# Kernel optimization log

Measured on AMD Instinct MI355X. Metric: run time of the kernel, lower is better.

The kernel has to match this reference:

```python
import jax, jax.numpy as jnp
import numpy as np

SAMPLE_RATE = 44100.0


def _peaking_coeffs(freq, gain_db, q, fs):
    """RBJ cookbook peaking-EQ biquad coefficients (as in dasp-pytorch).
    freq/gain_db/q: [B, K]. Returns normalized b0,b1,b2,a1,a2 each [B, K]."""
    A = jnp.power(10.0, gain_db / 40.0)
    w0 = 2.0 * jnp.pi * freq / fs
    cosw = jnp.cos(w0)
    alpha = jnp.sin(w0) / (2.0 * q)
    b0 = 1.0 + alpha * A
    b1 = -2.0 * cosw
    b2 = 1.0 - alpha * A
    a0 = 1.0 + alpha / A
    a1 = -2.0 * cosw
    a2 = 1.0 - alpha / A
    inv_a0 = 1.0 / a0
    return b0 * inv_a0, b1 * inv_a0, b2 * inv_a0, a1 * inv_a0, a2 * inv_a0


def setup_inputs() -> dict:
    key = jax.random.key(0)
    k1, k2, k3, k4 = jax.random.split(key, 4)
    B, C, T, K = 32, 2, 262144, 6
    audio = jax.random.normal(k1, (B, C, T), dtype=jnp.float32) * 0.1
    # realistic EQ parameter ranges
    frequencies = 100.0 + jax.random.uniform(k2, (B, K), dtype=jnp.float32) * 9900.0  # 100 Hz .. 10 kHz
    gains = jax.random.normal(k3, (B, K), dtype=jnp.float32) * 6.0                     # ~ +/- 6 dB
    q_factors = 0.5 + jax.random.uniform(k4, (B, K), dtype=jnp.float32) * 3.0          # 0.5 .. 3.5
    return {"audio": audio, "frequencies": frequencies, "gains": gains, "q_factors": q_factors}


def reference(audio, frequencies, gains, q_factors):
    # audio: [B, C, T]; per-batch cascade of K peaking biquads over time.
    B, C, T = audio.shape
    K = frequencies.shape[1]
    b0, b1, b2, a1, a2 = _peaking_coeffs(frequencies, gains, q_factors, SAMPLE_RATE)
    # [K, B, 1] for broadcasting over channels
    b0, b1, b2, a1, a2 = (jnp.transpose(c)[:, :, None] for c in (b0, b1, b2, a1, a2))

    def step(carry, x):  # x: [B, C], one time sample through the whole cascade
        s1, s2 = carry  # each [K, B, C], direct-form II transposed states
        y = x
        ns1, ns2 = [], []
        for k in range(K):  # small fixed band loop (structurally sequential cascade)
            yk = b0[k] * y + s1[k]
            ns1.append(b1[k] * y - a1[k] * yk + s2[k])
            ns2.append(b2[k] * y - a2[k] * yk)
            y = yk
        return (jnp.stack(ns1), jnp.stack(ns2)), y

    init = (jnp.zeros((K, B, C), audio.dtype), jnp.zeros((K, B, C), audio.dtype))
    xs = jnp.moveaxis(audio, 2, 0)  # [T, B, C]
    _, ys = jax.lax.scan(step, init, xs)
    return jnp.moveaxis(ys, 0, 2)  # [B, C, T]
```

## Files before the change

kernel.cpp:

```cpp
#include <hip/hip_runtime.h>
#include <math.h>

namespace {
constexpr int B = 32, C = 2, T = 262144, K = 6;
constexpr int SEG = 2048;
constexpr int L = T / SEG;
constexpr int NBC = B * C;
constexpr int NST = 2 * K;
constexpr int LOG2L = 7;
constexpr int TS = 16;
constexpr int NT = L / TS;
constexpr int WPB = SEG / 64;
constexpr int GP = 8;
constexpr int NW = 4;
constexpr float FS = 44100.0f;
}

__device__ __forceinline__ float rl(float v, int lane) {
  return __int_as_float(__builtin_amdgcn_readlane(__float_as_int(v), lane));
}

__device__ __forceinline__ void ld12(const float* p, float (&v)[NST]) {
  const float4* q = reinterpret_cast<const float4*>(p);
  float4 a = q[0], b4 = q[1], c4 = q[2];
  v[0] = a.x; v[1] = a.y; v[2] = a.z; v[3] = a.w;
  v[4] = b4.x; v[5] = b4.y; v[6] = b4.z; v[7] = b4.w;
  v[8] = c4.x; v[9] = c4.y; v[10] = c4.z; v[11] = c4.w;
}

__device__ __forceinline__ void st12(float* p, const float (&v)[NST]) {
  float4* q = reinterpret_cast<float4*>(p);
  q[0] = make_float4(v[0], v[1], v[2], v[3]);
  q[1] = make_float4(v[4], v[5], v[6], v[7]);
  q[2] = make_float4(v[8], v[9], v[10], v[11]);
}

__device__ __forceinline__ void affine(const float (&M)[NST][NST], float (&s)[NST],
                                       const float (&z)[NST]) {
  float ns[NST];
#pragma unroll
  for (int r = 0; r < NST; ++r) {
    float a = z[r];
#pragma unroll
    for (int m = 0; m < NST; ++m) a = fmaf(M[r][m], s[m], a);
    ns[r] = a;
  }
#pragma unroll
  for (int r = 0; r < NST; ++r) s[r] = ns[r];
}

__device__ __forceinline__ void coeffs_for_b(const float* __restrict__ fr,
                                             const float* __restrict__ gn,
                                             const float* __restrict__ qf, int b,
                                             float (&cb0)[K], float (&cb1)[K],
                                             float (&cb2)[K], float (&ca1)[K],
                                             float (&ca2)[K]) {
#pragma unroll
  for (int k = 0; k < K; ++k) {
    float f = fr[b * K + k], g = gn[b * K + k], Q = qf[b * K + k];
    float A  = powf(10.0f, g * (1.0f / 40.0f));
    float w0 = 6.283185307179586f * f / FS;
    float cw = cosf(w0);
    float al = sinf(w0) / (2.0f * Q);
    float ia = 1.0f / (1.0f + al / A);
    cb0[k] = (1.0f + al * A) * ia;
    cb1[k] = (-2.0f * cw) * ia;
    cb2[k] = (1.0f - al * A) * ia;
    ca1[k] = (-2.0f * cw) * ia;
    ca2[k] = (1.0f - al / A) * ia;
  }
}

template <bool WRITE_OUT>
__global__ __launch_bounds__(64, 2) void eq_pass(const float* __restrict__ x,
                                                 const float* __restrict__ fr,
                                                 const float* __restrict__ gn,
                                                 const float* __restrict__ qf,
                                                 float* __restrict__ cf,
                                                 const float* __restrict__ st_in,
                                                 float* __restrict__ st_out,
                                                 float* __restrict__ y) {
  __shared__ float sIn[2][64][17];
  __shared__ float sOut[2][64][17];

  int l = threadIdx.x;
  int wid = blockIdx.x;
  int bc = wid / WPB;
  int segbase = (wid % WPB) * 64;
  int b = bc / C;
  int tid = bc * SEG + segbase + l;

  const float4* xp4 = reinterpret_cast<const float4*>(x + (size_t)bc * T + (size_t)segbase * L);
  float4* yp4 = reinterpret_cast<float4*>(y + (size_t)bc * T + (size_t)segbase * L);
  constexpr int Q4 = L / 4;

  int sj = l >> 2;
  int qj = l & 3;

  float4 ra[4], rb[4];
#pragma unroll
  for (int j = 0; j < 4; ++j) ra[j] = xp4[(size_t)(j * 16 + sj) * Q4 + qj];
#pragma unroll
  for (int j = 0; j < 4; ++j) rb[j] = xp4[(size_t)(j * 16 + sj) * Q4 + 4 + qj];

  float b0[K], b1c[K], b2c[K], a1c[K], a2c[K];
  if (!WRITE_OUT) {
    coeffs_for_b(fr, gn, qf, b, b0, b1c, b2c, a1c, a2c);
    if ((wid % (WPB * C)) == 0) {
#pragma unroll
      for (int k = 0; k < K; ++k) {
        if (l == k) {
          float* p = cf + (b * K + k) * 5;
          p[0] = b0[k]; p[1] = b1c[k]; p[2] = b2c[k]; p[3] = a1c[k]; p[4] = a2c[k];
        }
      }
    }
  } else {
#pragma unroll
    for (int k = 0; k < K; ++k) {
      const float* p = cf + (b * K + k) * 5;
      b0[k] = p[0]; b1c[k] = p[1]; b2c[k] = p[2]; a1c[k] = p[3]; a2c[k] = p[4];
    }
  }

  float s1[K], s2[K];
  if (WRITE_OUT) {
    float st[NST];
    ld12(st_in + (size_t)tid * NST, st);
#pragma unroll
    for (int k = 0; k < K; ++k) { s1[k] = st[2 * k]; s2[k] = st[2 * k + 1]; }
  } else {
#pragma unroll
    for (int k = 0; k < K; ++k) { s1[k] = 0.0f; s2[k] = 0.0f; }
  }

  auto tile = [&](float4 (&r)[4], int t, int pb) {
#pragma unroll
    for (int j = 0; j < 4; ++j) {
      int seg = j * 16 + sj;
      sIn[pb][seg][qj * 4 + 0] = r[j].x;
      sIn[pb][seg][qj * 4 + 1] = r[j].y;
      sIn[pb][seg][qj * 4 + 2] = r[j].z;
      sIn[pb][seg][qj * 4 + 3] = r[j].w;
    }
    if (t + 2 < NT) {
#pragma unroll
      for (int j = 0; j < 4; ++j)
        r[j] = xp4[(size_t)(j * 16 + sj) * Q4 + (size_t)(t + 2) * 4 + qj];
    }
    float out16[TS];
#pragma unroll
    for (int i = 0; i < TS; ++i) {
      float yv = sIn[pb][l][i];
#pragma unroll
      for (int k = 0; k < K; ++k) {
        float yk = fmaf(b0[k], yv, s1[k]);
        float t1 = fmaf(b1c[k], yv, s2[k]);
        s1[k] = fmaf(-a1c[k], yk, t1);
        float t2 = b2c[k] * yv;
        s2[k] = fmaf(-a2c[k], yk, t2);
        yv = yk;
      }
      out16[i] = yv;
    }
    if (WRITE_OUT) {
#pragma unroll
      for (int i = 0; i < TS; ++i) sOut[pb][l][i] = out16[i];
#pragma unroll
      for (int j = 0; j < 4; ++j) {
        int seg = j * 16 + sj;
        float4 o;
        o.x = sOut[pb][seg][qj * 4 + 0];
        o.y = sOut[pb][seg][qj * 4 + 1];
        o.z = sOut[pb][seg][qj * 4 + 2];
        o.w = sOut[pb][seg][qj * 4 + 3];
        yp4[(size_t)seg * Q4 + (size_t)t * 4 + qj] = o;
      }
    }
  };

  for (int tt = 0; tt < NT; tt += 2) {
    tile(ra, tt, 0);
    tile(rb, tt + 1, 1);
  }

  if (!WRITE_OUT) {
    float st[NST];
#pragma unroll
    for (int k = 0; k < K; ++k) { st[2 * k] = s1[k]; st[2 * k + 1] = s2[k]; }
    st12(st_out + (size_t)tid * NST, st);
  }
}

__global__ __launch_bounds__(256, 1) void eq_scan(const float* __restrict__ cf,
                                                  const float* __restrict__ zsf,
                                                  float* __restrict__ sif) {
  __shared__ float PhiL[NST][NST];
  __shared__ float Rg[NST][NST + 1];
  __shared__ float Rw[NST][NST + 1];
  __shared__ float FB[NW][64][NST + 1];
  __shared__ float SL[NW][64][NST + 1];
  __shared__ float WF[NW][NST + 1];

  int bc = blockIdx.x;
  int b = bc / C;
  int t = threadIdx.x;
  int w = t >> 6;
  int l = t & 63;
  bool act = (l < NST);

  float b0[K], b1c[K], b2c[K], a1c[K], a2c[K];
#pragma unroll
  for (int k = 0; k < K; ++k) {
    const float* p = cf + (b * K + k) * 5;
    b0[k] = p[0]; b1c[k] = p[1]; b2c[k] = p[2]; a1c[k] = p[3]; a2c[k] = p[4];
  }

  float col[NST];
  {
    float s1[K], s2[K];
#pragma unroll
    for (int k = 0; k < K; ++k) {
      s1[k] = (l == 2 * k) ? 1.0f : 0.0f;
      s2[k] = (l == 2 * k + 1) ? 1.0f : 0.0f;
    }
    float yv = 0.0f;
#pragma unroll
    for (int k = 0; k < K; ++k) {
      float yk = fmaf(b0[k], yv, s1[k]);
      float t1 = fmaf(b1c[k], yv, s2[k]);
      float ns1 = fmaf(-a1c[k], yk, t1);
      float ns2 = fmaf(-a2c[k], yk, b2c[k] * yv);
      s1[k] = ns1; s2[k] = ns2; yv = yk;
    }
#pragma unroll
    for (int k = 0; k < K; ++k) { col[2 * k] = s1[k]; col[2 * k + 1] = s2[k]; }
  }

  auto square = [&]() {
    float nc[NST];
#pragma unroll
    for (int r = 0; r < NST; ++r) nc[r] = 0.0f;
#pragma unroll
    for (int m = 0; m < NST; ++m) {
      float wv = col[m];
#pragma unroll
      for (int r = 0; r < NST; ++r) nc[r] = fmaf(rl(col[r], m), wv, nc[r]);
    }
#pragma unroll
    for (int r = 0; r < NST; ++r) col[r] = nc[r];
  };

  for (int p = 0; p < LOG2L; ++p) square();
  if (w == 0 && act) {
#pragma unroll
    for (int r = 0; r < NST; ++r) PhiL[r][l] = col[r];
  }
  for (int p = 0; p < 3; ++p) square();
  if (w == 0 && act) {
#pragma unroll
    for (int r = 0; r < NST; ++r) Rg[r][l] = col[r];
  }
  for (int p = 0; p < 6; ++p) square();
  if (w == 0 && act) {
#pragma unroll
    for (int r = 0; r < NST; ++r) Rw[r][l] = col[r];
  }
  __syncthreads();

  float rowg[NST], roww[NST];
#pragma unroll
  for (int m = 0; m < NST; ++m) {
    rowg[m] = act ? Rg[l][m] : 0.0f;
    roww[m] = act ? Rw[l][m] : 0.0f;
  }
  float phi[NST][NST];
#pragma unroll
  for (int r = 0; r < NST; ++r)
#pragma unroll
    for (int m = 0; m < NST; ++m) phi[r][m] = PhiL[r][m];

  const float* zb = zsf + ((size_t)bc * SEG + (size_t)t * GP) * NST;
  float s[NST];
  ld12(zb, s);
#pragma unroll
  for (int j = 1; j < GP; ++j) {
    float zc[NST];
    ld12(zb + (size_t)j * NST, zc);
    affine(phi, s, zc);
  }
#pragma unroll
  for (int r = 0; r < NST; ++r) FB[w][l][r] = s[r];
  __syncthreads();

  {
    float sv = 0.0f;
    for (int i = 0; i < 64; ++i) {
      float wv = act ? FB[w][i][l] : 0.0f;
      float t0 = fmaf(rowg[0], rl(sv, 0), fmaf(rowg[1], rl(sv, 1), rowg[2] * rl(sv, 2)));
      float t1 = fmaf(rowg[3], rl(sv, 3), fmaf(rowg[4], rl(sv, 4), rowg[5] * rl(sv, 5)));
      float t2 = fmaf(rowg[6], rl(sv, 6), fmaf(rowg[7], rl(sv, 7), rowg[8] * rl(sv, 8)));
      float t3 = fmaf(rowg[9], rl(sv, 9), fmaf(rowg[10], rl(sv, 10), rowg[11] * rl(sv, 11)));
      sv = ((t0 + t1) + (t2 + t3)) + wv;
    }
    if (act) WF[w][l] = sv;
  }
  __syncthreads();

  float swv = 0.0f;
  for (int w2 = 0; w2 < w; ++w2) {
    float wfv = act ? WF[w2][l] : 0.0f;
    float t0 = fmaf(roww[0], rl(swv, 0), fmaf(roww[1], rl(swv, 1), roww[2] * rl(swv, 2)));
    float t1 = fmaf(roww[3], rl(swv, 3), fmaf(roww[4], rl(swv, 4), roww[5] * rl(swv, 5)));
    float t2 = fmaf(roww[6], rl(swv, 6), fmaf(roww[7], rl(swv, 7), roww[8] * rl(swv, 8)));
    float t3 = fmaf(roww[9], rl(swv, 9), fmaf(roww[10], rl(swv, 10), roww[11] * rl(swv, 11)));
    swv = ((t0 + t1) + (t2 + t3)) + wfv;
  }

  {
    float sv = swv;
    for (int i = 0; i < 64; ++i) {
      if (act) SL[w][i][l] = sv;
      float wv = act ? FB[w][i][l] : 0.0f;
      float t0 = fmaf(rowg[0], rl(sv, 0), fmaf(rowg[1], rl(sv, 1), rowg[2] * rl(sv, 2)));
      float t1 = fmaf(rowg[3], rl(sv, 3), fmaf(rowg[4], rl(sv, 4), rowg[5] * rl(sv, 5)));
      float t2 = fmaf(rowg[6], rl(sv, 6), fmaf(rowg[7], rl(sv, 7), rowg[8] * rl(sv, 8)));
      float t3 = fmaf(rowg[9], rl(sv, 9), fmaf(rowg[10], rl(sv, 10), rowg[11] * rl(sv, 11)));
      sv = ((t0 + t1) + (t2 + t3)) + wv;
    }
  }
  __syncthreads();

  float sg[NST];
#pragma unroll
  for (int r = 0; r < NST; ++r) sg[r] = SL[w][l][r];
  float* ob = sif + ((size_t)bc * SEG + (size_t)t * GP) * NST;
#pragma unroll
  for (int j = 0; j < GP; ++j) {
    st12(ob + (size_t)j * NST, sg);
    if (j + 1 < GP) {
      float zc[NST];
      ld12(zb + (size_t)j * NST, zc);
      affine(phi, sg, zc);
    }
  }
}

extern "C" void kernel_launch(void* const* d_in, const int* in_sizes, int n_in,
                              void* d_out, int out_size, void* d_ws, size_t ws_size,
                              hipStream_t stream) {
  const float* audio = (const float*)d_in[0];
  const float* fr    = (const float*)d_in[1];
  const float* gn    = (const float*)d_in[2];
  const float* qf    = (const float*)d_in[3];
  float* out = (float*)d_out;

  float* cf  = (float*)d_ws;
  float* zsf = cf + B * K * 5;
  float* sif = zsf + (size_t)NBC * SEG * NST;

  hipLaunchKernelGGL((eq_pass<false>), dim3(NBC * WPB), dim3(64), 0, stream,
                     audio, fr, gn, qf, cf, nullptr, zsf, out);
  hipLaunchKernelGGL(eq_scan, dim3(NBC), dim3(256), 0, stream, cf, zsf, sif);
  hipLaunchKernelGGL((eq_pass<true>), dim3(NBC * WPB), dim3(64), 0, stream,
                     audio, fr, gn, qf, cf, sif, nullptr, out);
}
```

Measured before the change: 84.44 us.

## Fuse two-pass scan into single kernel with decoupled lookback across blocks

Replaces the three-kernel scheme (local pass writing per-segment states, a separate scan kernel, and a second pass) with a small prep kernel computing coefficients and transition-matrix powers, plus one fused kernel. Each block handles one chunk of a row, does the local zero-state pass, an in-block scan of segment states, and then waits on a flag from the previous chunk's block to chain inter-block carries before rerunning the filter and writing output. This removes the global write and read of all per-segment states and two kernel boundaries, but serializes chunks through spin-waiting flags and relies on all blocks of a row being co-resident to avoid stalls.

```diff
diff --git a/kernel.cpp b/kernel.cpp
--- a/kernel.cpp
+++ b/kernel.cpp
@@ -3,58 +3,48 @@
 
 namespace {
 constexpr int B = 32, C = 2, T = 262144, K = 6;
-constexpr int SEG = 2048;
-constexpr int L = T / SEG;
 constexpr int NBC = B * C;
 constexpr int NST = 2 * K;
-constexpr int LOG2L = 7;
+constexpr int PB = 8;
+constexpr int CH = T / PB;
+constexpr int NW = 4;
+constexpr int SEGL = CH / (NW * 64);
 constexpr int TS = 16;
-constexpr int NT = L / TS;
-constexpr int WPB = SEG / 64;
-constexpr int GP = 8;
-constexpr int NW = 4;
+constexpr int NT = SEGL / TS;
+constexpr int Q4 = SEGL / 4;
+constexpr int SQ1 = 7;
+constexpr int SQ2 = 6;
+constexpr int SQ3 = 2;
 constexpr float FS = 44100.0f;
+constexpr size_t OFF_CF = 0;
+constexpr size_t OFF_RL = 960;
+constexpr size_t OFF_RW = OFF_RL + 4608;
+constexpr size_t OFF_RC = OFF_RW + 4608;
+constexpr size_t OFF_ST = OFF_RC + 4608;
+constexpr size_t OFF_FL = OFF_ST + 6144;
 }
 
 __device__ __forceinline__ float rl(float v, int lane) {
   return __int_as_float(__builtin_amdgcn_readlane(__float_as_int(v), lane));
 }
 
-__device__ __forceinline__ void ld12(const float* p, float (&v)[NST]) {
-  const float4* q = reinterpret_cast<const float4*>(p);
-  float4 a = q[0], b4 = q[1], c4 = q[2];
-  v[0] = a.x; v[1] = a.y; v[2] = a.z; v[3] = a.w;
-  v[4] = b4.x; v[5] = b4.y; v[6] = b4.z; v[7] = b4.w;
-  v[8] = c4.x; v[9] = c4.y; v[10] = c4.z; v[11] = c4.w;
-}
-
-__device__ __forceinline__ void st12(float* p, const float (&v)[NST]) {
-  float4* q = reinterpret_cast<float4*>(p);
-  q[0] = make_float4(v[0], v[1], v[2], v[3]);
-  q[1] = make_float4(v[4], v[5], v[6], v[7]);
-  q[2] = make_float4(v[8], v[9], v[10], v[11]);
-}
-
-__device__ __forceinline__ void affine(const float (&M)[NST][NST], float (&s)[NST],
-                                       const float (&z)[NST]) {
-  float ns[NST];
-#pragma unroll
-  for (int r = 0; r < NST; ++r) {
-    float a = z[r];
-#pragma unroll
-    for (int m = 0; m < NST; ++m) a = fmaf(M[r][m], s[m], a);
-    ns[r] = a;
-  }
-#pragma unroll
-  for (int r = 0; r < NST; ++r) s[r] = ns[r];
-}
-
-__device__ __forceinline__ void coeffs_for_b(const float* __restrict__ fr,
-                                             const float* __restrict__ gn,
-                                             const float* __restrict__ qf, int b,
-                                             float (&cb0)[K], float (&cb1)[K],
-                                             float (&cb2)[K], float (&ca1)[K],
-                                             float (&ca2)[K]) {
+__device__ __forceinline__ float mv_step(const float (&row)[NST], float sv) {
+  float t0 = fmaf(row[0], rl(sv, 0), fmaf(row[1], rl(sv, 1), row[2] * rl(sv, 2)));
+  float t1 = fmaf(row[3], rl(sv, 3), fmaf(row[4], rl(sv, 4), row[5] * rl(sv, 5)));
+  float t2 = fmaf(row[6], rl(sv, 6), fmaf(row[7], rl(sv, 7), row[8] * rl(sv, 8)));
+  float t3 = fmaf(row[9], rl(sv, 9), fmaf(row[10], rl(sv, 10), row[11] * rl(sv, 11)));
+  return (t0 + t1) + (t2 + t3);
+}
+
+__global__ __launch_bounds__(64) void eq_prep(const float* __restrict__ fr,
+                                              const float* __restrict__ gn,
+                                              const float* __restrict__ qf,
+                                              float* __restrict__ ws) {
+  int b = blockIdx.x;
+  int l = threadIdx.x;
+  float* cf = ws + OFF_CF;
+
+  float cb0[K], cb1[K], cb2[K], ca1[K], ca2[K];
 #pragma unroll
   for (int k = 0; k < K; ++k) {
     float f = fr[b * K + k], g = gn[b * K + k], Q = qf[b * K + k];
@@ -69,280 +59,272 @@
     ca1[k] = (-2.0f * cw) * ia;
     ca2[k] = (1.0f - al / A) * ia;
   }
-}
-
-template <bool WRITE_OUT>
-__global__ __launch_bounds__(64, 2) void eq_pass(const float* __restrict__ x,
-                                                 const float* __restrict__ fr,
-                                                 const float* __restrict__ gn,
-                                                 const float* __restrict__ qf,
-                                                 float* __restrict__ cf,
-                                                 const float* __restrict__ st_in,
-                                                 float* __restrict__ st_out,
-                                                 float* __restrict__ y) {
-  __shared__ float sIn[2][64][17];
-  __shared__ float sOut[2][64][17];
-
-  int l = threadIdx.x;
-  int wid = blockIdx.x;
-  int bc = wid / WPB;
-  int segbase = (wid % WPB) * 64;
-  int b = bc / C;
-  int tid = bc * SEG + segbase + l;
-
-  const float4* xp4 = reinterpret_cast<const float4*>(x + (size_t)bc * T + (size_t)segbase * L);
-  float4* yp4 = reinterpret_cast<float4*>(y + (size_t)bc * T + (size_t)segbase * L);
-  constexpr int Q4 = L / 4;
-
-  int sj = l >> 2;
-  int qj = l & 3;
+#pragma unroll
+  for (int k = 0; k < K; ++k) {
+    if (l == k) {
+      float* p = cf + (b * K + k) * 5;
+      p[0] = cb0[k]; p[1] = cb1[k]; p[2] = cb2[k]; p[3] = ca1[k]; p[4] = ca2[k];
+    }
+  }
+
+  float col[NST];
+  {
+    float s1[K], s2[K];
+#pragma unroll
+    for (int k = 0; k < K; ++k) {
+      s1[k] = (l == 2 * k) ? 1.0f : 0.0f;
+      s2[k] = (l == 2 * k + 1) ? 1.0f : 0.0f;
+    }
+    float yv = 0.0f;
+#pragma unroll
+    for (int k = 0; k < K; ++k) {
+      float yk = fmaf(cb0[k], yv, s1[k]);
+      float t1 = fmaf(cb1[k], yv, s2[k]);
+      float ns1 = fmaf(-ca1[k], yk, t1);
+      float ns2 = fmaf(-ca2[k], yk, cb2[k] * yv);
+      s1[k] = ns1; s2[k] = ns2; yv = yk;
+    }
+#pragma unroll
+    for (int k = 0; k < K; ++k) { col[2 * k] = s1[k]; col[2 * k + 1] = s2[k]; }
+  }
+
+  auto square = [&]() {
+    float nc[NST];
+#pragma unroll
+    for (int r = 0; r < NST; ++r) nc[r] = 0.0f;
+#pragma unroll
+    for (int m = 0; m < NST; ++m) {
+      float wv = col[m];
+#pragma unroll
+      for (int r = 0; r < NST; ++r) nc[r] = fmaf(rl(col[r], m), wv, nc[r]);
+    }
+#pragma unroll
+    for (int r = 0; r < NST; ++r) col[r] = nc[r];
+  };
+  auto dump = [&](float* G) {
+    if (l < NST) {
+#pragma unroll
+      for (int r = 0; r < NST; ++r) G[(size_t)b * 144 + r * 12 + l] = col[r];
+    }
+  };
+
+  for (int p = 0; p < SQ1; ++p) square();
+  dump(ws + OFF_RL);
+  for (int p = 0; p < SQ2; ++p) square();
+  dump(ws + OFF_RW);
+  for (int p = 0; p < SQ3; ++p) square();
+  dump(ws + OFF_RC);
+}
+
+__global__ __launch_bounds__(256, 2) void eq_fused(const float* __restrict__ x,
+                                                   float* __restrict__ ws,
+                                                   float* __restrict__ y) {
+  __shared__ float P1[NW][2][64][17];
+  __shared__ float U[NW * 2 * 64 * 17];
+  __shared__ float BIN[16];
+
+  const float* cf = ws + OFF_CF;
+  float* states = ws + OFF_ST;
+  unsigned* flags = (unsigned*)(ws + OFF_FL);
+
+  int t = threadIdx.x, w = t >> 6, l = t & 63;
+  int blk = blockIdx.x, row = blk / PB, p = blk % PB, b = row >> 1;
+  bool act = (l < NST);
+
+  auto FBp = [&](int ww, int i, int r) -> float& { return U[(ww * 64 + i) * 13 + r]; };
+  auto SLp = [&](int ww, int i, int r) -> float& { return U[3328 + (ww * 64 + i) * 13 + r]; };
+  auto WFp = [&](int ww, int r) -> float& { return U[6656 + ww * 13 + r]; };
+  auto SO = [&](int pb, int seg, int c) -> float& { return U[((w * 2 + pb) * 64 + seg) * 17 + c]; };
+
+  const float4* xq = reinterpret_cast<const float4*>(
+      x + (size_t)row * T + (size_t)p * CH + (size_t)w * (64 * SEGL));
+  float4* yq = reinterpret_cast<float4*>(
+      y + (size_t)row * T + (size_t)p * CH + (size_t)w * (64 * SEGL));
+
+  int sj = l >> 2, qj = l & 3;
 
   float4 ra[4], rb[4];
 #pragma unroll
-  for (int j = 0; j < 4; ++j) ra[j] = xp4[(size_t)(j * 16 + sj) * Q4 + qj];
-#pragma unroll
-  for (int j = 0; j < 4; ++j) rb[j] = xp4[(size_t)(j * 16 + sj) * Q4 + 4 + qj];
+  for (int j = 0; j < 4; ++j) ra[j] = xq[(size_t)(j * 16 + sj) * Q4 + qj];
+#pragma unroll
+  for (int j = 0; j < 4; ++j) rb[j] = xq[(size_t)(j * 16 + sj) * Q4 + 4 + qj];
 
   float b0[K], b1c[K], b2c[K], a1c[K], a2c[K];
-  if (!WRITE_OUT) {
-    coeffs_for_b(fr, gn, qf, b, b0, b1c, b2c, a1c, a2c);
-    if ((wid % (WPB * C)) == 0) {
-#pragma unroll
-      for (int k = 0; k < K; ++k) {
-        if (l == k) {
-          float* p = cf + (b * K + k) * 5;
-          p[0] = b0[k]; p[1] = b1c[k]; p[2] = b2c[k]; p[3] = a1c[k]; p[4] = a2c[k];
-        }
-      }
-    }
-  } else {
-#pragma unroll
-    for (int k = 0; k < K; ++k) {
-      const float* p = cf + (b * K + k) * 5;
-      b0[k] = p[0]; b1c[k] = p[1]; b2c[k] = p[2]; a1c[k] = p[3]; a2c[k] = p[4];
-    }
+#pragma unroll
+  for (int k = 0; k < K; ++k) {
+    const float* cp = cf + (b * K + k) * 5;
+    b0[k] = cp[0]; b1c[k] = cp[1]; b2c[k] = cp[2]; a1c[k] = cp[3]; a2c[k] = cp[4];
+  }
+  float rowL[NST], rowW[NST], rowC[NST];
+#pragma unroll
+  for (int m = 0; m < NST; ++m) {
+    rowL[m] = act ? ws[OFF_RL + (size_t)b * 144 + l * 12 + m] : 0.0f;
+    rowW[m] = act ? ws[OFF_RW + (size_t)b * 144 + l * 12 + m] : 0.0f;
+    rowC[m] = act ? ws[OFF_RC + (size_t)b * 144 + l * 12 + m] : 0.0f;
   }
 
   float s1[K], s2[K];
-  if (WRITE_OUT) {
-    float st[NST];
-    ld12(st_in + (size_t)tid * NST, st);
-#pragma unroll
-    for (int k = 0; k < K; ++k) { s1[k] = st[2 * k]; s2[k] = st[2 * k + 1]; }
-  } else {
-#pragma unroll
-    for (int k = 0; k < K; ++k) { s1[k] = 0.0f; s2[k] = 0.0f; }
-  }
-
-  auto tile = [&](float4 (&r)[4], int t, int pb) {
+#pragma unroll
+  for (int k = 0; k < K; ++k) { s1[k] = 0.0f; s2[k] = 0.0f; }
+
+  auto stage = [&](float4 (&r)[4], int pb) {
 #pragma unroll
     for (int j = 0; j < 4; ++j) {
       int seg = j * 16 + sj;
-      sIn[pb][seg][qj * 4 + 0] = r[j].x;
-      sIn[pb][seg][qj * 4 + 1] = r[j].y;
-      sIn[pb][seg][qj * 4 + 2] = r[j].z;
-      sIn[pb][seg][qj * 4 + 3] = r[j].w;
-    }
-    if (t + 2 < NT) {
+      P1[w][pb][seg][qj * 4 + 0] = r[j].x;
+      P1[w][pb][seg][qj * 4 + 1] = r[j].y;
+      P1[w][pb][seg][qj * 4 + 2] = r[j].z;
+      P1[w][pb][seg][qj * 4 + 3] = r[j].w;
+    }
+  };
+  auto prefetch = [&](float4 (&r)[4], int tnext) {
+    if (tnext < NT) {
 #pragma unroll
       for (int j = 0; j < 4; ++j)
-        r[j] = xp4[(size_t)(j * 16 + sj) * Q4 + (size_t)(t + 2) * 4 + qj];
-    }
-    float out16[TS];
+        r[j] = xq[(size_t)(j * 16 + sj) * Q4 + (size_t)tnext * 4 + qj];
+    }
+  };
+
+  for (int tt = 0; tt < NT; tt += 2) {
+    stage(ra, 0);
+    prefetch(ra, tt + 2);
 #pragma unroll
     for (int i = 0; i < TS; ++i) {
-      float yv = sIn[pb][l][i];
+      float yv = P1[w][0][l][i];
 #pragma unroll
       for (int k = 0; k < K; ++k) {
         float yk = fmaf(b0[k], yv, s1[k]);
         float t1 = fmaf(b1c[k], yv, s2[k]);
         s1[k] = fmaf(-a1c[k], yk, t1);
-        float t2 = b2c[k] * yv;
-        s2[k] = fmaf(-a2c[k], yk, t2);
+        s2[k] = fmaf(-a2c[k], yk, b2c[k] * yv);
         yv = yk;
       }
-      out16[i] = yv;
-    }
-    if (WRITE_OUT) {
-#pragma unroll
-      for (int i = 0; i < TS; ++i) sOut[pb][l][i] = out16[i];
-#pragma unroll
-      for (int j = 0; j < 4; ++j) {
-        int seg = j * 16 + sj;
-        float4 o;
-        o.x = sOut[pb][seg][qj * 4 + 0];
-        o.y = sOut[pb][seg][qj * 4 + 1];
-        o.z = sOut[pb][seg][qj * 4 + 2];
-        o.w = sOut[pb][seg][qj * 4 + 3];
-        yp4[(size_t)seg * Q4 + (size_t)t * 4 + qj] = o;
-      }
-    }
-  };
-
-  for (int tt = 0; tt < NT; tt += 2) {
-    tile(ra, tt, 0);
-    tile(rb, tt + 1, 1);
-  }
-
-  if (!WRITE_OUT) {
-    float st[NST];
-#pragma unroll
-    for (int k = 0; k < K; ++k) { st[2 * k] = s1[k]; st[2 * k + 1] = s2[k]; }
-    st12(st_out + (size_t)tid * NST, st);
-  }
-}
-
-__global__ __launch_bounds__(256, 1) void eq_scan(const float* __restrict__ cf,
-                                                  const float* __restrict__ zsf,
-                                                  float* __restrict__ sif) {
-  __shared__ float PhiL[NST][NST];
-  __shared__ float Rg[NST][NST + 1];
-  __shared__ float Rw[NST][NST + 1];
-  __shared__ float FB[NW][64][NST + 1];
-  __shared__ float SL[NW][64][NST + 1];
-  __shared__ float WF[NW][NST + 1];
-
-  int bc = blockIdx.x;
-  int b = bc / C;
-  int t = threadIdx.x;
-  int w = t >> 6;
-  int l = t & 63;
-  bool act = (l < NST);
-
-  float b0[K], b1c[K], b2c[K], a1c[K], a2c[K];
-#pragma unroll
-  for (int k = 0; k < K; ++k) {
-    const float* p = cf + (b * K + k) * 5;
-    b0[k] = p[0]; b1c[k] = p[1]; b2c[k] = p[2]; a1c[k] = p[3]; a2c[k] = p[4];
-  }
-
-  float col[NST];
-  {
-    float s1[K], s2[K];
-#pragma unroll
-    for (int k = 0; k < K; ++k) {
-      s1[k] = (l == 2 * k) ? 1.0f : 0.0f;
-      s2[k] = (l == 2 * k + 1) ? 1.0f : 0.0f;
-    }
-    float yv = 0.0f;
-#pragma unroll
-    for (int k = 0; k < K; ++k) {
-      float yk = fmaf(b0[k], yv, s1[k]);
-      float t1 = fmaf(b1c[k], yv, s2[k]);
-      float ns1 = fmaf(-a1c[k], yk, t1);
-      float ns2 = fmaf(-a2c[k], yk, b2c[k] * yv);
-      s1[k] = ns1; s2[k] = ns2; yv = yk;
-    }
-#pragma unroll
-    for (int k = 0; k < K; ++k) { col[2 * k] = s1[k]; col[2 * k + 1] = s2[k]; }
-  }
-
-  auto square = [&]() {
-    float nc[NST];
-#pragma unroll
-    for (int r = 0; r < NST; ++r) nc[r] = 0.0f;
-#pragma unroll
-    for (int m = 0; m < NST; ++m) {
-      float wv = col[m];
-#pragma unroll
-      for (int r = 0; r < NST; ++r) nc[r] = fmaf(rl(col[r], m), wv, nc[r]);
-    }
-#pragma unroll
-    for (int r = 0; r < NST; ++r) col[r] = nc[r];
-  };
-
-  for (int p = 0; p < LOG2L; ++p) square();
-  if (w == 0 && act) {
-#pragma unroll
-    for (int r = 0; r < NST; ++r) PhiL[r][l] = col[r];
-  }
-  for (int p = 0; p < 3; ++p) square();
-  if (w == 0 && act) {
-#pragma unroll
-    for (int r = 0; r < NST; ++r) Rg[r][l] = col[r];
-  }
-  for (int p = 0; p < 6; ++p) square();
-  if (w == 0 && act) {
-#pragma unroll
-    for (int r = 0; r < NST; ++r) Rw[r][l] = col[r];
-  }
-  __syncthreads();
-
-  float rowg[NST], roww[NST];
-#pragma unroll
-  for (int m = 0; m < NST; ++m) {
-    rowg[m] = act ? Rg[l][m] : 0.0f;
-    roww[m] = act ? Rw[l][m] : 0.0f;
-  }
-  float phi[NST][NST];
-#pragma unroll
-  for (int r = 0; r < NST; ++r)
-#pragma unroll
-    for (int m = 0; m < NST; ++m) phi[r][m] = PhiL[r][m];
-
-  const float* zb = zsf + ((size_t)bc * SEG + (size_t)t * GP) * NST;
-  float s[NST];
-  ld12(zb, s);
-#pragma unroll
-  for (int j = 1; j < GP; ++j) {
-    float zc[NST];
-    ld12(zb + (size_t)j * NST, zc);
-    affine(phi, s, zc);
-  }
-#pragma unroll
-  for (int r = 0; r < NST; ++r) FB[w][l][r] = s[r];
+    }
+    stage(rb, 1);
+    prefetch(rb, tt + 3);
+#pragma unroll
+    for (int i = 0; i < TS; ++i) {
+      float yv = P1[w][1][l][i];
+#pragma unroll
+      for (int k = 0; k < K; ++k) {
+        float yk = fmaf(b0[k], yv, s1[k]);
+        float t1 = fmaf(b1c[k], yv, s2[k]);
+        s1[k] = fmaf(-a1c[k], yk, t1);
+        s2[k] = fmaf(-a2c[k], yk, b2c[k] * yv);
+        yv = yk;
+      }
+    }
+  }
+#pragma unroll
+  for (int k = 0; k < K; ++k) { FBp(w, l, 2 * k) = s1[k]; FBp(w, l, 2 * k + 1) = s2[k]; }
   __syncthreads();
 
   {
     float sv = 0.0f;
     for (int i = 0; i < 64; ++i) {
-      float wv = act ? FB[w][i][l] : 0.0f;
-      float t0 = fmaf(rowg[0], rl(sv, 0), fmaf(rowg[1], rl(sv, 1), rowg[2] * rl(sv, 2)));
-      float t1 = fmaf(rowg[3], rl(sv, 3), fmaf(rowg[4], rl(sv, 4), rowg[5] * rl(sv, 5)));
-      float t2 = fmaf(rowg[6], rl(sv, 6), fmaf(rowg[7], rl(sv, 7), rowg[8] * rl(sv, 8)));
-      float t3 = fmaf(rowg[9], rl(sv, 9), fmaf(rowg[10], rl(sv, 10), rowg[11] * rl(sv, 11)));
-      sv = ((t0 + t1) + (t2 + t3)) + wv;
-    }
-    if (act) WF[w][l] = sv;
+      float wv = act ? FBp(w, i, l) : 0.0f;
+      sv = mv_step(rowL, sv) + wv;
+    }
+    if (act) WFp(w, l) = sv;
   }
   __syncthreads();
 
-  float swv = 0.0f;
-  for (int w2 = 0; w2 < w; ++w2) {
-    float wfv = act ? WF[w2][l] : 0.0f;
-    float t0 = fmaf(roww[0], rl(swv, 0), fmaf(roww[1], rl(swv, 1), roww[2] * rl(swv, 2)));
-    float t1 = fmaf(roww[3], rl(swv, 3), fmaf(roww[4], rl(swv, 4), roww[5] * rl(swv, 5)));
-    float t2 = fmaf(roww[6], rl(swv, 6), fmaf(roww[7], rl(swv, 7), roww[8] * rl(swv, 8)));
-    float t3 = fmaf(roww[9], rl(swv, 9), fmaf(roww[10], rl(swv, 10), roww[11] * rl(swv, 11)));
-    swv = ((t0 + t1) + (t2 + t3)) + wfv;
-  }
+#pragma unroll
+  for (int j = 0; j < 4; ++j) ra[j] = xq[(size_t)(j * 16 + sj) * Q4 + qj];
+#pragma unroll
+  for (int j = 0; j < 4; ++j) rb[j] = xq[(size_t)(j * 16 + sj) * Q4 + 4 + qj];
+
+  if (w == 0) {
+    float bz = 0.0f;
+#pragma unroll
+    for (int w2 = 0; w2 < NW; ++w2) {
+      float wv = act ? WFp(w2, l) : 0.0f;
+      bz = mv_step(rowW, bz) + wv;
+    }
+    float bin = 0.0f;
+    if (p > 0) {
+      if (l == 0) {
+        while (atomicAdd(&flags[blk - 1], 0u) == 0u) { __builtin_amdgcn_s_sleep(8); }
+      }
+      __threadfence();
+      if (act) bin = atomicAdd(&states[(size_t)(blk - 1) * NST + l], 0.0f);
+    }
+    if (p < PB - 1) {
+      float bout = mv_step(rowC, bin) + bz;
+      if (act) atomicExch(&states[(size_t)blk * NST + l], bout);
+      __threadfence();
+      if (l == 0) atomicExch(&flags[blk], 1u);
+    }
+    if (act) BIN[l] = bin;
+  }
+  __syncthreads();
 
   {
-    float sv = swv;
+    float sv = act ? BIN[l] : 0.0f;
+    for (int w2 = 0; w2 < w; ++w2) {
+      float wv = act ? WFp(w2, l) : 0.0f;
+      sv = mv_step(rowW, sv) + wv;
+    }
     for (int i = 0; i < 64; ++i) {
-      if (act) SL[w][i][l] = sv;
-      float wv = act ? FB[w][i][l] : 0.0f;
-      float t0 = fmaf(rowg[0], rl(sv, 0), fmaf(rowg[1], rl(sv, 1), rowg[2] * rl(sv, 2)));
-      float t1 = fmaf(rowg[3], rl(sv, 3), fmaf(rowg[4], rl(sv, 4), rowg[5] * rl(sv, 5)));
-      float t2 = fmaf(rowg[6], rl(sv, 6), fmaf(rowg[7], rl(sv, 7), rowg[8] * rl(sv, 8)));
-      float t3 = fmaf(rowg[9], rl(sv, 9), fmaf(rowg[10], rl(sv, 10), rowg[11] * rl(sv, 11)));
-      sv = ((t0 + t1) + (t2 + t3)) + wv;
-    }
-  }
+      if (act) SLp(w, i, l) = sv;
+      float wv = act ? FBp(w, i, l) : 0.0f;
+      sv = mv_step(rowL, sv) + wv;
+    }
+  }
+  float st[NST];
+#pragma unroll
+  for (int r = 0; r < NST; ++r) st[r] = SLp(w, l, r);
   __syncthreads();
 
-  float sg[NST];
-#pragma unroll
-  for (int r = 0; r < NST; ++r) sg[r] = SL[w][l][r];
-  float* ob = sif + ((size_t)bc * SEG + (size_t)t * GP) * NST;
-#pragma unroll
-  for (int j = 0; j < GP; ++j) {
-    st12(ob + (size_t)j * NST, sg);
-    if (j + 1 < GP) {
-      float zc[NST];
-      ld12(zb + (size_t)j * NST, zc);
-      affine(phi, sg, zc);
-    }
+#pragma unroll
+  for (int k = 0; k < K; ++k) { s1[k] = st[2 * k]; s2[k] = st[2 * k + 1]; }
+
+  auto flush = [&](int pb, int tt) {
+#pragma unroll
+    for (int j = 0; j < 4; ++j) {
+      int seg = j * 16 + sj;
+      float4 o;
+      o.x = SO(pb, seg, qj * 4 + 0);
+      o.y = SO(pb, seg, qj * 4 + 1);
+      o.z = SO(pb, seg, qj * 4 + 2);
+      o.w = SO(pb, seg, qj * 4 + 3);
+      yq[(size_t)seg * Q4 + (size_t)tt * 4 + qj] = o;
+    }
+  };
+
+  for (int tt = 0; tt < NT; tt += 2) {
+    stage(ra, 0);
+    prefetch(ra, tt + 2);
+#pragma unroll
+    for (int i = 0; i < TS; ++i) {
+      float yv = P1[w][0][l][i];
+#pragma unroll
+      for (int k = 0; k < K; ++k) {
+        float yk = fmaf(b0[k], yv, s1[k]);
+        float t1 = fmaf(b1c[k], yv, s2[k]);
+        s1[k] = fmaf(-a1c[k], yk, t1);
+        s2[k] = fmaf(-a2c[k], yk, b2c[k] * yv);
+        yv = yk;
+      }
+      SO(0, l, i) = yv;
+    }
+    flush(0, tt);
+    stage(rb, 1);
+    prefetch(rb, tt + 3);
+#pragma unroll
+    for (int i = 0; i < TS; ++i) {
+      float yv = P1[w][1][l][i];
+#pragma unroll
+      for (int k = 0; k < K; ++k) {
+        float yk = fmaf(b0[k], yv, s1[k]);
+        float t1 = fmaf(b1c[k], yv, s2[k]);
+        s1[k] = fmaf(-a1c[k], yk, t1);
+        s2[k] = fmaf(-a2c[k], yk, b2c[k] * yv);
+        yv = yk;
+      }
+      SO(1, l, i) = yv;
+    }
+    flush(1, tt + 1);
   }
 }
 
@@ -354,14 +336,11 @@
   const float* gn    = (const float*)d_in[2];
   const float* qf    = (const float*)d_in[3];
   float* out = (float*)d_out;
-
-  float* cf  = (float*)d_ws;
-  float* zsf = cf + B * K * 5;
-  float* sif = zsf + (size_t)NBC * SEG * NST;
-
-  hipLaunchKernelGGL((eq_pass<false>), dim3(NBC * WPB), dim3(64), 0, stream,
-                     audio, fr, gn, qf, cf, nullptr, zsf, out);
-  hipLaunchKernelGGL(eq_scan, dim3(NBC), dim3(256), 0, stream, cf, zsf, sif);
-  hipLaunchKernelGGL((eq_pass<true>), dim3(NBC * WPB), dim3(64), 0, stream,
-                     audio, fr, gn, qf, cf, sif, nullptr, out);
-}
+  float* ws = (float*)d_ws;
+
+  hipMemsetAsync((char*)d_ws + OFF_FL * sizeof(float), 0,
+                 NBC * PB * sizeof(unsigned), stream);
+  hipLaunchKernelGGL(eq_prep, dim3(B), dim3(64), 0, stream, fr, gn, qf, ws);
+  hipLaunchKernelGGL(eq_fused, dim3(NBC * PB), dim3(256), 0, stream,
+                     audio, ws, out);
+}
```

New measurement: 135.7 us. 1.61x slower.
